# Kernel tuning notes

Measured on AMD Instinct MI355X. Metric: run time of the kernel, lower is better.

## Reference

```python
import jax, jax.numpy as jnp
import numpy as np

B, T, C, E, K, CAP, H = 8, 2048, 1024, 8, 2, 4096, 4096


def setup_inputs() -> dict:
    key = jax.random.key(0)
    ks = jax.random.split(key, 6)
    s = 0.02
    return {
        "x": jax.random.normal(ks[0], (B, T, C), jnp.float32),
        "rw1": s * jax.random.normal(ks[1], (C, H), jnp.float32),
        "rb1": jnp.zeros((H,), jnp.float32),
        "rw2": s * jax.random.normal(ks[2], (H, E), jnp.float32),
        "rb2": jnp.zeros((E,), jnp.float32),
        "ew1": s * jax.random.normal(ks[3], (E, C, H), jnp.float32),
        "eb1": jnp.zeros((E, H), jnp.float32),
        "ew2": s * jax.random.normal(ks[4], (E, H, C), jnp.float32),
        "eb2": jnp.zeros((E, C), jnp.float32),
    }


def reference(x, rw1, rb1, rw2, rb2, ew1, eb1, ew2, eb2):
    Bx, Tx, Cx = x.shape
    N = Bx * Tx
    # Router FFN -> gating logits [B,T,E]
    logits = jax.nn.relu(x @ rw1 + rb1) @ rw2 + rb2
    vals, ids = jax.lax.top_k(logits, K)           # [B,T,K]
    probs = jax.nn.softmax(vals, axis=-1)          # [B,T,K]

    ids_f = ids.reshape(N * K)                     # expert id per (token, k) slot
    probs_f = probs.reshape(N * K)
    xr = jnp.repeat(x.reshape(N, Cx), K, axis=0)   # [N*K, C], token order preserved

    # position of each slot within its expert's capacity buffer
    m = jax.nn.one_hot(ids_f, E, dtype=jnp.int32)  # [N*K, E]
    pos = jnp.cumsum(m, axis=0) - 1
    pos_tok = jnp.take_along_axis(pos, ids_f[:, None], axis=1)[:, 0]
    keep = (pos_tok < CAP).astype(x.dtype)         # drop tokens over capacity (padding)
    pos_c = jnp.clip(pos_tok, 0, CAP - 1)

    # dispatch: scatter tokens into per-expert padded buffers [E, CAP, C]
    disp = jnp.zeros((E, CAP, Cx), x.dtype).at[ids_f, pos_c].add(xr * keep[:, None])

    # expert FFN, batched over experts
    h = jax.nn.relu(jnp.einsum('enc,ech->enh', disp, ew1) + eb1[:, None, :])
    eo = jnp.einsum('enh,ehc->enc', h, ew2) + eb2[:, None, :]

    # combine: gather expert outputs back, weight by gate prob, sum over k
    y = eo[ids_f, pos_c] * (probs_f * keep)[:, None]   # [N*K, C]
    return y.reshape(Bx, Tx, K, Cx).sum(axis=2)
```

## Files before the change

### kernel.cpp

```cpp
#include <hip/hip_runtime.h>
#include <cstdint>
#include <type_traits>

#define B_    8
#define T_    2048
#define C_    1024
#define E_    8
#define K_    2
#define CAP_  4096
#define H_    4096
#define NTOK  (B_ * T_)
#define NSLOT (NTOK * K_)
#define KR_   3072

typedef __bf16 bf16x8 __attribute__((ext_vector_type(8)));
typedef float  f32x4  __attribute__((ext_vector_type(4)));

#define AS1 __attribute__((address_space(1)))
#define AS3 __attribute__((address_space(3)))

static __device__ __forceinline__ float b2f(unsigned short u) {
    union { float f; unsigned int i; } v; v.i = ((unsigned int)u) << 16; return v.f;
}
static __device__ __forceinline__ unsigned short f2b(float f) {
    unsigned int x = __float_as_uint(f);
    unsigned int r = (x + 0x7fffu + ((x >> 16) & 1u)) >> 16;
    return (unsigned short)r;
}

template<int W> static __device__ __forceinline__ void vm_wait() {
    if constexpr (W == 4) asm volatile("s_waitcnt vmcnt(4)" ::: "memory");
    else if constexpr (W == 0) asm volatile("s_waitcnt vmcnt(0)" ::: "memory");
}

template<int RELU, typename TC, int EPI>
__global__ __launch_bounds__(512, 2) void gemm256_8ph(
    const unsigned short* __restrict__ A, const unsigned short* __restrict__ BT,
    const float* __restrict__ bias, TC* __restrict__ Cout,
    int Kd, int Nld, int NT,
    long rabA, long rabB,
    long thrA, long thrB,
    long sA, long sB, long sBias, long sC,
    const float* __restrict__ rw2v, float* __restrict__ plogv)
{
    extern __shared__ char smem[];

    const int z = blockIdx.z;
    A    += (size_t)z * sA;
    BT   += (size_t)z * sB;
    bias += (size_t)z * sBias;
    if constexpr (EPI == 0) Cout += (size_t)z * sC;

    const int gx = gridDim.x;
    const int nwg = gx * gridDim.y;
    int wg = blockIdx.y * gx + blockIdx.x;
    wg = (wg & 7) * (nwg >> 3) + (wg >> 3);
    const int bm = (wg / gx) * 256;
    const int bn = (wg % gx) * 256;

    const int tid  = threadIdx.x;
    const int lane = tid & 63;
    const int wid  = tid >> 6;
    const int wrow = (wid >> 2) * 128;
    const int wcol = (wid & 3) * 64;
    const int fr = lane & 15;
    const int fq = lane >> 4;

    const char* Ag = (const char*)A  + (size_t)bm * rabA;
    const char* Bg = (const char*)BT + (size_t)bn * rabB;

    f32x4 acc[8][4];
#pragma unroll
    for (int i = 0; i < 8; i++)
#pragma unroll
        for (int j = 0; j < 4; j++) acc[i][j] = (f32x4){0.f, 0.f, 0.f, 0.f};

    auto STAGE_A = [&](int kt) {
        char* d = smem + (size_t)(kt & 1) * 65536;
        long kb = (long)kt * 128;
        if (kb >= thrA) kb -= thrA;
#pragma unroll
        for (int r = 0; r < 4; ++r) {
            const int o    = r * 8192 + tid * 16;
            const int row  = o >> 7;
            const int slot = (o >> 4) & 7;
            const int ss   = (slot ^ (row & 7)) << 4;
            __builtin_amdgcn_global_load_lds(
                (const AS1 void*)(Ag + (size_t)row * rabA + kb + ss),
                (AS3 void*)(d + r * 8192 + wid * 1024), 16, 0, 0);
        }
    };
    auto STAGE_B = [&](int kt) {
        char* d = smem + (size_t)(kt & 1) * 65536 + 32768;
        long kb = (long)kt * 128;
        if (kb >= thrB) kb -= thrB;
#pragma unroll
        for (int r = 0; r < 4; ++r) {
            const int o    = r * 8192 + tid * 16;
            const int row  = o >> 7;
            const int slot = (o >> 4) & 7;
            const int ss   = (slot ^ (row & 7)) << 4;
            __builtin_amdgcn_global_load_lds(
                (const AS1 void*)(Bg + (size_t)row * rabB + kb + ss),
                (AS3 void*)(d + r * 8192 + wid * 1024), 16, 0, 0);
        }
    };

    auto LDA = [&](int kt, int mi, int kk) -> bf16x8 {
        const char* base = smem + (size_t)(kt & 1) * 65536;
        const int row  = wrow + mi * 16 + fr;
        const int slot = (kk * 4 + fq) ^ (row & 7);
        return *(const bf16x8*)(base + row * 128 + slot * 16);
    };
    auto LDB = [&](int kt, int ni, int kk) -> bf16x8 {
        const char* base = smem + (size_t)(kt & 1) * 65536 + 32768;
        const int row  = wcol + ni * 16 + fr;
        const int slot = (kk * 4 + fq) ^ (row & 7);
        return *(const bf16x8*)(base + row * 128 + slot * 16);
    };

    STAGE_A(0); STAGE_B(0); STAGE_B(1);
    vm_wait<4>();
    __builtin_amdgcn_s_barrier();

    bf16x8 a[4], bb[4];
    for (int kt = 0; kt < NT; ++kt) {
#pragma unroll
        for (int i = 0; i < 4; ++i) a[i]  = LDA(kt, i, 0);
#pragma unroll
        for (int i = 0; i < 4; ++i) bb[i] = LDB(kt, i, 0);
        if (kt + 1 < NT) STAGE_A(kt + 1);
        __builtin_amdgcn_s_barrier();
        __builtin_amdgcn_s_setprio(1);
#pragma unroll
        for (int mi = 0; mi < 4; ++mi)
#pragma unroll
            for (int ni = 0; ni < 4; ++ni)
                acc[mi][ni] = __builtin_amdgcn_mfma_f32_16x16x32_bf16(
                    a[mi], bb[ni], acc[mi][ni], 0, 0, 0);
        __builtin_amdgcn_s_setprio(0);
        __builtin_amdgcn_s_barrier();
#pragma unroll
        for (int i = 0; i < 4; ++i) a[i] = LDA(kt, 4 + i, 0);
        __builtin_amdgcn_s_barrier();
        __builtin_amdgcn_s_setprio(1);
#pragma unroll
        for (int mi = 0; mi < 4; ++mi)
#pragma unroll
            for (int ni = 0; ni < 4; ++ni)
                acc[4 + mi][ni] = __builtin_amdgcn_mfma_f32_16x16x32_bf16(
                    a[mi], bb[ni], acc[4 + mi][ni], 0, 0, 0);
        __builtin_amdgcn_s_setprio(0);
        __builtin_amdgcn_s_barrier();
#pragma unroll
        for (int i = 0; i < 4; ++i) a[i]  = LDA(kt, i, 1);
#pragma unroll
        for (int i = 0; i < 4; ++i) bb[i] = LDB(kt, i, 1);
        __builtin_amdgcn_s_barrier();
        __builtin_amdgcn_s_setprio(1);
#pragma unroll
        for (int mi = 0; mi < 4; ++mi)
#pragma unroll
            for (int ni = 0; ni < 4; ++ni)
                acc[mi][ni] = __builtin_amdgcn_mfma_f32_16x16x32_bf16(
                    a[mi], bb[ni], acc[mi][ni], 0, 0, 0);
        __builtin_amdgcn_s_setprio(0);
        __builtin_amdgcn_s_barrier();
#pragma unroll
        for (int i = 0; i < 4; ++i) a[i] = LDA(kt, 4 + i, 1);
        if (kt + 2 < NT) STAGE_B(kt + 2);
        if (kt + 1 < NT) {
            if (kt + 2 < NT) vm_wait<4>();
            else             vm_wait<0>();
        }
        __builtin_amdgcn_s_barrier();
        __builtin_amdgcn_s_setprio(1);
#pragma unroll
        for (int mi = 0; mi < 4; ++mi)
#pragma unroll
            for (int ni = 0; ni < 4; ++ni)
                acc[4 + mi][ni] = __builtin_amdgcn_mfma_f32_16x16x32_bf16(
                    a[mi], bb[ni], acc[4 + mi][ni], 0, 0, 0);
        __builtin_amdgcn_s_setprio(0);
        __builtin_amdgcn_s_barrier();
    }

    const float* bias_o = bias;
    asm volatile("" : "+s"(bias_o));

    if constexpr (EPI == 3) {
        float w2r[4][8];
#pragma unroll
        for (int ni = 0; ni < 4; ++ni) {
            const float* src = rw2v + (size_t)(bn + wcol + ni * 16 + fr) * 8;
            *(float4*)(w2r[ni])     = *(const float4*)(src);
            *(float4*)(w2r[ni] + 4) = *(const float4*)(src + 4);
        }
        float bv[4];
#pragma unroll
        for (int ni = 0; ni < 4; ++ni)
            bv[ni] = bias_o[bn + wcol + ni * 16 + fr];

        float* pb = (float*)smem;
        const int rowhalf = wid >> 2, colwave = wid & 3;
        const int frq = fr >> 2;

#pragma unroll
        for (int mi = 0; mi < 8; ++mi) {
#pragma unroll
            for (int rg = 0; rg < 4; ++rg) {
                float p[8];
#pragma unroll
                for (int e = 0; e < 8; ++e) p[e] = 0.f;
#pragma unroll
                for (int ni = 0; ni < 4; ++ni) {
                    const float h = fmaxf(acc[mi][ni][rg] + bv[ni], 0.f);
#pragma unroll
                    for (int e = 0; e < 8; ++e) p[e] = fmaf(h, w2r[ni][e], p[e]);
                }
#pragma unroll
                for (int e = 0; e < 8; ++e) {
                    p[e] += __shfl_xor(p[e], 1);
                    p[e] += __shfl_xor(p[e], 2);
                }
                if ((fr & 3) == 0) {
                    const int row = mi * 16 + fq * 4 + rg;
                    float* dst = pb +
                        ((((size_t)rowhalf * 4 + colwave) * 128 + row) * 4 + frq) * 8;
                    *(float4*)(dst)     = make_float4(p[0], p[1], p[2], p[3]);
                    *(float4*)(dst + 4) = make_float4(p[4], p[5], p[6], p[7]);
                }
            }
        }
        __syncthreads();
        {
            const int r  = tid >> 1;
            const int eh = (tid & 1) * 4;
            const int rowhalf2 = r >> 7, rl = r & 127;
            float4 s = make_float4(0.f, 0.f, 0.f, 0.f);
#pragma unroll
            for (int cw = 0; cw < 4; ++cw)
#pragma unroll
                for (int q = 0; q < 4; ++q) {
                    const float4 v = *(const float4*)(pb +
                        ((((size_t)rowhalf2 * 4 + cw) * 128 + rl) * 4 + q) * 8 + eh);
                    s.x += v.x; s.y += v.y; s.z += v.z; s.w += v.w;
                }
            *(float4*)(plogv + ((size_t)(bn >> 8) * NTOK + bm + r) * 8 + eh) = s;
        }
    } else {
#pragma unroll
        for (int mi = 0; mi < 8; ++mi) {
#pragma unroll
            for (int ni = 0; ni < 4; ++ni) {
                const int c = bn + wcol + ni * 16 + fr;
                const float bv = bias_o[c];
#pragma unroll
                for (int rg = 0; rg < 4; ++rg) {
                    const int r = bm + wrow + mi * 16 + fq * 4 + rg;
                    float v = acc[mi][ni][rg] + bv;
                    if (RELU) v = fmaxf(v, 0.f);
                    if constexpr (std::is_same_v<TC, float>)
                        Cout[(size_t)r * Nld + c] = v;
                    else
                        Cout[(size_t)r * Nld + c] = f2b(v);
                }
            }
        }
    }
}

__global__ __launch_bounds__(256) void router_topk_final(
    const float* __restrict__ plog, const float* __restrict__ rb2,
    int* __restrict__ ids, float* __restrict__ probs)
{
    const int n = blockIdx.x * 256 + threadIdx.x;
    float l[E_];
#pragma unroll
    for (int e = 0; e < E_; ++e) l[e] = rb2[e];
#pragma unroll
    for (int bx = 0; bx < 16; ++bx) {
        const float4 a = *(const float4*)(plog + ((size_t)bx * NTOK + n) * 8);
        const float4 b = *(const float4*)(plog + ((size_t)bx * NTOK + n) * 8 + 4);
        l[0] += a.x; l[1] += a.y; l[2] += a.z; l[3] += a.w;
        l[4] += b.x; l[5] += b.y; l[6] += b.z; l[7] += b.w;
    }
    float v1 = -1e30f, v2 = -1e30f; int i1 = 0, i2 = 0;
#pragma unroll
    for (int e = 0; e < E_; ++e) {
        const float v = l[e];
        if (v > v1)      { v2 = v1; i2 = i1; v1 = v; i1 = e; }
        else if (v > v2) { v2 = v;  i2 = e; }
    }
    const float e2 = expf(v2 - v1);
    const float inv = 1.f / (1.f + e2);
    ids[n * 2] = i1;  ids[n * 2 + 1] = i2;
    probs[n * 2] = inv; probs[n * 2 + 1] = e2 * inv;
}

__global__ __launch_bounds__(256) void split_x(
    const float* __restrict__ x, unsigned short* __restrict__ A2)
{
    const int n = blockIdx.x;
    const int c = threadIdx.x * 4;
    const float4 v = *(const float4*)(x + (size_t)n * C_ + c);
    ushort4 hi, lo;
    hi.x = f2b(v.x); lo.x = f2b(v.x - b2f(hi.x));
    hi.y = f2b(v.y); lo.y = f2b(v.y - b2f(hi.y));
    hi.z = f2b(v.z); lo.z = f2b(v.z - b2f(hi.z));
    hi.w = f2b(v.w); lo.w = f2b(v.w - b2f(hi.w));
    unsigned short* row = A2 + (size_t)n * 2048;
    *(ushort4*)(row + c)        = hi;
    *(ushort4*)(row + C_ + c)   = lo;
}

__global__ __launch_bounds__(256) void split_w(
    const float* __restrict__ in, unsigned short* __restrict__ out)
{
    __shared__ float t[32][33];
    const int rb = blockIdx.y * 32;
    const int cb = blockIdx.x * 32;
    const int tr = threadIdx.x >> 3, tc = (threadIdx.x & 7) * 4;
    const float4 v = *(const float4*)(in + (size_t)(rb + tr) * H_ + cb + tc);
    t[tr][tc + 0] = v.x; t[tr][tc + 1] = v.y; t[tr][tc + 2] = v.z; t[tr][tc + 3] = v.w;
    __syncthreads();
    ushort4 hi, lo;
    float f;
    f = t[tc + 0][tr]; hi.x = f2b(f); lo.x = f2b(f - b2f(hi.x));
    f = t[tc + 1][tr]; hi.y = f2b(f); lo.y = f2b(f - b2f(hi.y));
    f = t[tc + 2][tr]; hi.z = f2b(f); lo.z = f2b(f - b2f(hi.z));
    f = t[tc + 3][tr]; hi.w = f2b(f); lo.w = f2b(f - b2f(hi.w));
    unsigned short* row = out + (size_t)(cb + tr) * 2048;
    *(ushort4*)(row + rb + tc)        = hi;
    *(ushort4*)(row + C_ + rb + tc)   = lo;
}

__global__ __launch_bounds__(256) void transpose_cvt(
    const float* __restrict__ in, unsigned short* __restrict__ out, int R, int Ncols)
{
    __shared__ float t[32][33];
    const size_t zoff = (size_t)blockIdx.z * R * Ncols;
    in  += zoff;
    out += zoff;
    const int rb = blockIdx.y * 32, cb = blockIdx.x * 32;
    const int tr = threadIdx.x >> 3, tc = (threadIdx.x & 7) * 4;
    const float4 v = *(const float4*)(in + (size_t)(rb + tr) * Ncols + cb + tc);
    t[tr][tc + 0] = v.x; t[tr][tc + 1] = v.y; t[tr][tc + 2] = v.z; t[tr][tc + 3] = v.w;
    __syncthreads();
    ushort4 u;
    u.x = f2b(t[tc + 0][tr]); u.y = f2b(t[tc + 1][tr]);
    u.z = f2b(t[tc + 2][tr]); u.w = f2b(t[tc + 3][tr]);
    *(ushort4*)(out + (size_t)(cb + tr) * R + rb + tc) = u;
}

__global__ __launch_bounds__(1024) void compute_pos(
    const int* __restrict__ ids, int* __restrict__ pos)
{
    __shared__ int hist[1024][E_];
    const int t = threadIdx.x;
    const int per = NSLOT / 1024;
    int cnt[E_];
#pragma unroll
    for (int e = 0; e < E_; e++) cnt[e] = 0;
    const int s0 = t * per;
    for (int i = 0; i < per; i++) cnt[ids[s0 + i]]++;
#pragma unroll
    for (int e = 0; e < E_; e++) hist[t][e] = cnt[e];
    __syncthreads();
    const int wv = t >> 6, ln = t & 63;
    if (wv < E_) {
        const int e = wv;
        const int base = ln * 16;
        int vals[16];
        int s = 0;
#pragma unroll
        for (int i = 0; i < 16; i++) vals[i] = hist[base + i][e];
#pragma unroll
        for (int i = 0; i < 16; i++) { const int v = vals[i]; vals[i] = s; s += v; }
        int x = s;
        for (int d = 1; d < 64; d <<= 1) {
            const int y = __shfl_up(x, d);
            if (ln >= d) x += y;
        }
        const int excl = x - s;
#pragma unroll
        for (int i = 0; i < 16; i++) hist[base + i][e] = vals[i] + excl;
    }
    __syncthreads();
    int run[E_];
#pragma unroll
    for (int e = 0; e < E_; e++) run[e] = hist[t][e];
    for (int i = 0; i < per; i++) { const int e = ids[s0 + i]; pos[s0 + i] = run[e]++; }
}

__global__ __launch_bounds__(256) void dispatch_k(
    const float* __restrict__ x, const int* __restrict__ ids,
    const int* __restrict__ pos, unsigned short* __restrict__ disp)
{
    const int s = blockIdx.x;
    const int e = ids[s], p = pos[s];
    if (p >= CAP_) return;
    const int n = s >> 1;
    const float4 v = *(const float4*)(x + (size_t)n * C_ + threadIdx.x * 4);
    ushort4 u;
    u.x = f2b(v.x); u.y = f2b(v.y); u.z = f2b(v.z); u.w = f2b(v.w);
    *(ushort4*)(disp + ((size_t)e * CAP_ + p) * C_ + threadIdx.x * 4) = u;
}

__global__ __launch_bounds__(256) void combine_k(
    const unsigned short* __restrict__ eo, const int* __restrict__ ids,
    const int* __restrict__ pos, const float* __restrict__ probs,
    float* __restrict__ y)
{
    const int n = blockIdx.x;
    const int c = threadIdx.x * 4;
    float r0 = 0.f, r1 = 0.f, r2 = 0.f, r3 = 0.f;
#pragma unroll
    for (int k = 0; k < K_; k++) {
        const int p = pos[2 * n + k];
        if (p >= CAP_) continue;
        const int e = ids[2 * n + k];
        const float w = probs[2 * n + k];
        const ushort4 u = *(const ushort4*)(eo + ((size_t)e * CAP_ + p) * C_ + c);
        r0 = fmaf(w, b2f(u.x), r0); r1 = fmaf(w, b2f(u.y), r1);
        r2 = fmaf(w, b2f(u.z), r2); r3 = fmaf(w, b2f(u.w), r3);
    }
    *(float4*)(y + (size_t)n * C_ + c) = make_float4(r0, r1, r2, r3);
}

extern "C" void kernel_launch(void* const* d_in, const int* in_sizes, int n_in,
                              void* d_out, int out_size, void* d_ws, size_t ws_size,
                              hipStream_t stream)
{
    const float* x   = (const float*)d_in[0];
    const float* rw1 = (const float*)d_in[1];
    const float* rb1 = (const float*)d_in[2];
    const float* rw2 = (const float*)d_in[3];
    const float* rb2 = (const float*)d_in[4];
    const float* ew1 = (const float*)d_in[5];
    const float* eb1 = (const float*)d_in[6];
    const float* ew2 = (const float*)d_in[7];
    const float* eb2 = (const float*)d_in[8];
    float* y = (float*)d_out;

    char* ws = (char*)d_ws;
    unsigned short* hexp  = (unsigned short*)ws;
    unsigned short* A2    = (unsigned short*)(ws + 268435456L);
    unsigned short* disp  = (unsigned short*)(ws + 268435456L);
    unsigned short* eo    = (unsigned short*)(ws + 268435456L);
    unsigned short* BTW   = (unsigned short*)(ws + 335544320L);
    unsigned short* B2    = (unsigned short*)(ws + 369098752L);
    float*          plog  = (float*)(ws + 394264576L);
    int*            ids   = (int*)  (ws + 402653184L);
    float*          probs = (float*)(ws + 402784256L);
    int*            pos   = (int*)  (ws + 402915328L);

    const size_t LDSB = 131072;
    const long HUGE_ = 1L << 60;

    split_x<<<NTOK, 256, 0, stream>>>(x, A2);
    {
        dim3 g(H_ / 32, C_ / 32, 1);
        split_w<<<g, 256, 0, stream>>>(rw1, B2);
    }
    {
        dim3 g(H_ / 256, NTOK / 256, 1);
        gemm256_8ph<1, float, 3><<<g, 512, LDSB, stream>>>(
            A2, B2, rb1, (float*)nullptr, KR_, H_, KR_ / 64,
            4096 , 4096 , 4096 , 2048 ,
            0, 0, 0, 0, rw2, plog);
    }
    router_topk_final<<<NTOK / 256, 256, 0, stream>>>(plog, rb2, ids, probs);
    compute_pos<<<1, 1024, 0, stream>>>(ids, pos);
    dispatch_k<<<NSLOT, 256, 0, stream>>>(x, ids, pos, disp);
    {
        dim3 g(H_ / 32, C_ / 32, E_);
        transpose_cvt<<<g, 256, 0, stream>>>(ew1, BTW, C_, H_);
    }
    {
        dim3 g(H_ / 256, CAP_ / 256, E_);
        gemm256_8ph<1, unsigned short, 0><<<g, 512, LDSB, stream>>>(
            disp, BTW, eb1, hexp, C_, H_, C_ / 64,
            (long)C_ * 2, (long)C_ * 2, HUGE_, HUGE_,
            (long)CAP_ * C_, (long)H_ * C_, (long)H_, (long)CAP_ * H_,
            nullptr, nullptr);
    }
    {
        dim3 g(C_ / 32, H_ / 32, E_);
        transpose_cvt<<<g, 256, 0, stream>>>(ew2, BTW, H_, C_);
    }
    {
        dim3 g(C_ / 256, CAP_ / 256, E_);
        gemm256_8ph<0, unsigned short, 0><<<g, 512, LDSB, stream>>>(
            hexp, BTW, eb2, eo, H_, C_, H_ / 64,
            (long)H_ * 2, (long)H_ * 2, HUGE_, HUGE_,
            (long)CAP_ * H_, (long)C_ * H_, (long)C_, (long)CAP_ * C_,
            nullptr, nullptr);
    }
    combine_k<<<NTOK, 256, 0, stream>>>(eo, ids, pos, probs, y);
}
```

Before: 1.072 ms.

## Replace expert GEMMs with a smaller 128x256 double-buffered MFMA kernel

Adds a new gemm128n kernel using 128x256 output tiles, 256 threads, a K-step of 32 and a two-stage LDS double buffer fed by global_load_lds with XOR swizzling. Both expert FFN GEMMs now use it in place of the 256x256 eight-phase kernel, cutting LDS from 128KB to 48KB per block and doubling the block count. This is meant to raise occupancy and improve load balance across CUs. The trade-off is less data reuse per tile and a simpler pipeline that waits on all loads each K step.

```diff
diff --git a/kernel.cpp b/kernel.cpp
--- a/kernel.cpp
+++ b/kernel.cpp
@@ -33,13 +33,136 @@
     else if constexpr (W == 0) asm volatile("s_waitcnt vmcnt(0)" ::: "memory");
 }
 
+template<int RELU, typename TC>
+__global__ __launch_bounds__(256, 2) void gemm128n(
+    const unsigned short* __restrict__ A, const unsigned short* __restrict__ BT,
+    const float* __restrict__ bias, TC* __restrict__ Cout,
+    int Kd, int Nld, int NT,
+    long sA, long sB, long sBias, long sC)
+{
+    extern __shared__ char smem[];
+
+    const int z = blockIdx.z;
+    A    += (size_t)z * sA;
+    BT   += (size_t)z * sB;
+    bias += (size_t)z * sBias;
+    Cout += (size_t)z * sC;
+
+    const int gx = gridDim.x;
+    const int nwg = gx * gridDim.y;
+    int wg = blockIdx.y * gx + blockIdx.x;
+    wg = (wg & 7) * (nwg >> 3) + (wg >> 3);
+    const int bm = (wg / gx) * 128;
+    const int bn = (wg % gx) * 256;
+
+    const int tid  = threadIdx.x;
+    const int lane = tid & 63;
+    const int wid  = tid >> 6;
+    const int wrow = (wid >> 1) * 64;
+    const int wcol = (wid & 1) * 128;
+    const int fr = lane & 15;
+    const int fq = lane >> 4;
+
+    const size_t rbA = (size_t)Kd * 2;
+    const char* Ag = (const char*)A  + (size_t)bm * rbA;
+    const char* Bg = (const char*)BT + (size_t)bn * rbA;
+
+    f32x4 acc[4][8];
+#pragma unroll
+    for (int i = 0; i < 4; i++)
+#pragma unroll
+        for (int j = 0; j < 8; j++) acc[i][j] = (f32x4){0.f, 0.f, 0.f, 0.f};
+
+    auto STAGE = [&](int kt) {
+        char* dA = smem + (size_t)(kt & 1) * 24576;
+        char* dB = dA + 8192;
+        const size_t kb = (size_t)kt * 64;
+#pragma unroll
+        for (int r = 0; r < 2; ++r) {
+            const int o    = r * 4096 + tid * 16;
+            const int row  = o >> 6;
+            const int slot = (o >> 4) & 3;
+            const int ss   = (slot ^ (row & 3)) << 4;
+            __builtin_amdgcn_global_load_lds(
+                (const AS1 void*)(Ag + (size_t)row * rbA + kb + ss),
+                (AS3 void*)(dA + r * 4096 + wid * 1024), 16, 0, 0);
+        }
+#pragma unroll
+        for (int r = 0; r < 4; ++r) {
+            const int o    = r * 4096 + tid * 16;
+            const int row  = o >> 6;
+            const int slot = (o >> 4) & 3;
+            const int ss   = (slot ^ (row & 3)) << 4;
+            __builtin_amdgcn_global_load_lds(
+                (const AS1 void*)(Bg + (size_t)row * rbA + kb + ss),
+                (AS3 void*)(dB + r * 4096 + wid * 1024), 16, 0, 0);
+        }
+    };
+
+    auto COMPUTE = [&](int kt) {
+        const char* bufA = smem + (size_t)(kt & 1) * 24576;
+        const char* bufB = bufA + 8192;
+        bf16x8 a_[4], b_[8];
+#pragma unroll
+        for (int mi = 0; mi < 4; ++mi) {
+            const int row = wrow + mi * 16 + fr;
+            a_[mi] = *(const bf16x8*)(bufA + row * 64 + ((fq ^ (row & 3)) << 4));
+        }
+#pragma unroll
+        for (int ni = 0; ni < 8; ++ni) {
+            const int row = wcol + ni * 16 + fr;
+            b_[ni] = *(const bf16x8*)(bufB + row * 64 + ((fq ^ (row & 3)) << 4));
+        }
+        __builtin_amdgcn_s_setprio(1);
+#pragma unroll
+        for (int mi = 0; mi < 4; ++mi)
+#pragma unroll
+            for (int ni = 0; ni < 8; ++ni)
+                acc[mi][ni] = __builtin_amdgcn_mfma_f32_16x16x32_bf16(
+                    a_[mi], b_[ni], acc[mi][ni], 0, 0, 0);
+        __builtin_amdgcn_s_setprio(0);
+    };
+
+    STAGE(0);
+    vm_wait<0>();
+    __builtin_amdgcn_s_barrier();
+
+    for (int kt = 0; kt < NT - 1; ++kt) {
+        STAGE(kt + 1);
+        COMPUTE(kt);
+        vm_wait<0>();
+        __builtin_amdgcn_s_barrier();
+    }
+    COMPUTE(NT - 1);
+
+    const float* bias_o = bias;
+    asm volatile("" : "+s"(bias_o));
+#pragma unroll
+    for (int mi = 0; mi < 4; ++mi) {
+#pragma unroll
+        for (int ni = 0; ni < 8; ++ni) {
+            const int c = bn + wcol + ni * 16 + fr;
+            const float bv = bias_o[c];
+#pragma unroll
+            for (int rg = 0; rg < 4; ++rg) {
+                const int r = bm + wrow + mi * 16 + fq * 4 + rg;
+                float v = acc[mi][ni][rg] + bv;
+                if (RELU) v = fmaxf(v, 0.f);
+                if constexpr (std::is_same_v<TC, float>)
+                    Cout[(size_t)r * Nld + c] = v;
+                else
+                    Cout[(size_t)r * Nld + c] = f2b(v);
+            }
+        }
+    }
+}
+
 template<int RELU, typename TC, int EPI>
 __global__ __launch_bounds__(512, 2) void gemm256_8ph(
     const unsigned short* __restrict__ A, const unsigned short* __restrict__ BT,
     const float* __restrict__ bias, TC* __restrict__ Cout,
     int Kd, int Nld, int NT,
-    long rabA, long rabB,
-    long thrA, long thrB,
+    long rabA, long rabB, long thrA, long thrB,
     long sA, long sB, long sBias, long sC,
     const float* __restrict__ rw2v, float* __restrict__ plogv)
 {
@@ -455,8 +578,8 @@
     float*          probs = (float*)(ws + 402784256L);
     int*            pos   = (int*)  (ws + 402915328L);
 
-    const size_t LDSB = 131072;
-    const long HUGE_ = 1L << 60;
+    const size_t LDSR = 131072;
+    const size_t LDSE = 49152;
 
     split_x<<<NTOK, 256, 0, stream>>>(x, A2);
     {
@@ -465,10 +588,9 @@
     }
     {
         dim3 g(H_ / 256, NTOK / 256, 1);
-        gemm256_8ph<1, float, 3><<<g, 512, LDSB, stream>>>(
+        gemm256_8ph<1, float, 3><<<g, 512, LDSR, stream>>>(
             A2, B2, rb1, (float*)nullptr, KR_, H_, KR_ / 64,
-            4096 , 4096 , 4096 , 2048 ,
-            0, 0, 0, 0, rw2, plog);
+            4096, 4096, 4096, 2048, 0, 0, 0, 0, rw2, plog);
     }
     router_topk_final<<<NTOK / 256, 256, 0, stream>>>(plog, rb2, ids, probs);
     compute_pos<<<1, 1024, 0, stream>>>(ids, pos);
@@ -478,24 +600,20 @@
         transpose_cvt<<<g, 256, 0, stream>>>(ew1, BTW, C_, H_);
     }
     {
-        dim3 g(H_ / 256, CAP_ / 256, E_);
-        gemm256_8ph<1, unsigned short, 0><<<g, 512, LDSB, stream>>>(
-            disp, BTW, eb1, hexp, C_, H_, C_ / 64,
-            (long)C_ * 2, (long)C_ * 2, HUGE_, HUGE_,
-            (long)CAP_ * C_, (long)H_ * C_, (long)H_, (long)CAP_ * H_,
-            nullptr, nullptr);
+        dim3 g(H_ / 256, CAP_ / 128, E_);
+        gemm128n<1, unsigned short><<<g, 256, LDSE, stream>>>(
+            disp, BTW, eb1, hexp, C_, H_, C_ / 32,
+            (long)CAP_ * C_, (long)H_ * C_, (long)H_, (long)CAP_ * H_);
     }
     {
         dim3 g(C_ / 32, H_ / 32, E_);
         transpose_cvt<<<g, 256, 0, stream>>>(ew2, BTW, H_, C_);
     }
     {
-        dim3 g(C_ / 256, CAP_ / 256, E_);
-        gemm256_8ph<0, unsigned short, 0><<<g, 512, LDSB, stream>>>(
-            hexp, BTW, eb2, eo, H_, C_, H_ / 64,
-            (long)H_ * 2, (long)H_ * 2, HUGE_, HUGE_,
-            (long)CAP_ * H_, (long)C_ * H_, (long)C_, (long)CAP_ * C_,
-            nullptr, nullptr);
+        dim3 g(C_ / 256, CAP_ / 128, E_);
+        gemm128n<0, unsigned short><<<g, 256, LDSE, stream>>>(
+            hexp, BTW, eb2, eo, H_, C_, H_ / 32,
+            (long)CAP_ * H_, (long)C_ * H_, (long)C_, (long)CAP_ * C_);
     }
     combine_k<<<NTOK, 256, 0, stream>>>(eo, ids, pos, probs, y);
 }
```

Result: slower. 1.139 ms (+6.3%).
